# Kernel optimization log

Hardware: AMD Instinct MI355X
Metric: run time of the kernel (lower is better)

## Reference

```python
import jax, jax.numpy as jnp
import numpy as np


def _gelu(x):
    # torch.nn.functional.gelu default: exact erf form
    return jax.nn.gelu(x, approximate=False)


def setup_inputs() -> dict:
    key = jax.random.key(0)
    ks = jax.random.split(key, 6)
    B, L, H, MAXLEN = 8, 2048, 1024, 256
    former_input = jax.random.normal(ks[0], (B, L, H), dtype=jnp.float32)
    hidden_sates = jax.random.normal(ks[1], (B, L, H), dtype=jnp.float32)
    token_type_ids = jax.random.randint(ks[2], (B, L), 0, MAXLEN, dtype=jnp.int32)
    attention_mask = jnp.ones((B, L), dtype=jnp.float32)
    # learned params (init.normal_ std=0.02, biases zero)
    W_down = jax.random.normal(ks[3], (2 * H, H), dtype=jnp.float32) * 0.02
    b_down = jnp.zeros((H,), dtype=jnp.float32)
    W_row = jax.random.normal(ks[4], (H, H), dtype=jnp.float32) * 0.02
    b_row = jnp.zeros((H,), dtype=jnp.float32)
    return {
        "former_input": former_input,
        "hidden_sates": hidden_sates,
        "token_type_ids": token_type_ids,
        "attention_mask": attention_mask,
        "W_down": W_down,
        "b_down": b_down,
        "W_row": W_row,
        "b_row": b_row,
        "max_length": 256,
    }


def reference(former_input, hidden_sates, token_type_ids, attention_mask,
              W_down, b_down, W_row, b_row, max_length):
    # down_proj + gelu: [B, L, 2H] @ [2H, H] -> [B, L, H]
    x = jnp.concatenate([former_input, hidden_sates], axis=-1)
    sequence_output = _gelu(jnp.einsum("blf,fh->blh", x, W_down) + b_down)

    # one_hot_from @ sequence_output == segment-sum of tokens into table cells
    # cell_hidden[b, t] = sum_{l : token_type_ids[b,l]==t} sequence_output[b, l]
    seg = jax.vmap(lambda vals, ids: jax.ops.segment_sum(vals, ids, num_segments=max_length))
    cell_hidden = seg(sequence_output, token_type_ids)  # [B, max_length, H]

    # row_linear + gelu (dropout is identity in eval mode)
    cell_hidden = _gelu(jnp.einsum("bth,hk->btk", cell_hidden, W_row) + b_row)

    # one_hot_to @ cell_hidden == gather cell back to each token position
    seq_hidden = jnp.take_along_axis(
        cell_hidden, token_type_ids[:, :, None].astype(jnp.int32), axis=1
    )  # [B, L, H]
    return seq_hidden
```

## Files before the change

### kernel.cpp

```cpp
#include <hip/hip_runtime.h>

typedef unsigned short ushort_t;
typedef __bf16 bf16x8 __attribute__((ext_vector_type(8)));
typedef float f32x4 __attribute__((ext_vector_type(4)));

__device__ __forceinline__ unsigned short f2bf(float f) {
    unsigned u = __float_as_uint(f);
    u += 0x7fffu + ((u >> 16) & 1u);
    return (unsigned short)(u >> 16);
}
__device__ __forceinline__ float bf2f(unsigned short h) {
    return __uint_as_float(((unsigned)h) << 16);
}
__device__ __forceinline__ float gelu_f(float x) {
    return 0.5f * x * (1.0f + erff(x * 0.70710678118654752440f));
}

__global__ void prep_kernel(const float4* __restrict__ former,
                            const float4* __restrict__ hidden,
                            uint4* __restrict__ Xb4,
                            const float* __restrict__ Wd, ushort_t* __restrict__ WdT,
                            const float* __restrict__ Wr, ushort_t* __restrict__ WrT)
{
    const int blk = blockIdx.x;
    const int tid = threadIdx.x;
    if (blk < 16384) {
        const int row = blk;
        const float4* src = (tid < 128)
            ? (former + (size_t)row * 256 + (tid & 127) * 2)
            : (hidden + (size_t)row * 256 + (tid & 127) * 2);
        float4 a = src[0], b = src[1];
        uint4 o;
        o.x = f2bf(a.x) | ((unsigned)f2bf(a.y) << 16);
        o.y = f2bf(a.z) | ((unsigned)f2bf(a.w) << 16);
        o.z = f2bf(b.x) | ((unsigned)f2bf(b.y) << 16);
        o.w = f2bf(b.z) | ((unsigned)f2bf(b.w) << 16);
        Xb4[(size_t)row * 256 + tid] = o;
    } else {
        __shared__ float tile[32][33];
        const float* W; ushort_t* Wt; int R, C, b;
        if (blk < 16384 + 2048) { b = blk - 16384; W = Wd; Wt = WdT; R = 2048; C = 1024; }
        else                    { b = blk - 18432; W = Wr; Wt = WrT; R = 1024; C = 1024; }
        const int bx = (b & 31) * 32;
        const int by = (b >> 5) * 32;
        const int tx = tid & 31, ty = tid >> 5;
        #pragma unroll
        for (int j = 0; j < 32; j += 8)
            tile[ty + j][tx] = W[(size_t)(by + ty + j) * C + bx + tx];
        __syncthreads();
        #pragma unroll
        for (int j = 0; j < 32; j += 8)
            Wt[(size_t)(bx + ty + j) * R + by + tx] = f2bf(tile[tx][ty + j]);
    }
}

template <bool OUT_BF16>
__global__ void gemm_bias_gelu_kernel(const ushort_t* __restrict__ A,
                                      const ushort_t* __restrict__ Bt,
                                      const float* __restrict__ bias,
                                      void* __restrict__ C,
                                      int M, int N, int K)
{
    __shared__ __align__(16) ushort_t sA[128 * 64];
    __shared__ __align__(16) ushort_t sB[128 * 64];
    const int tid  = threadIdx.x;
    const int lane = tid & 63;
    const int wave = tid >> 6;
    const int wm = (wave & 1) * 64;
    const int wn = (wave >> 1) * 64;
    const long bm = (long)blockIdx.x * 128;
    const long bn = (long)blockIdx.y * 128;

    f32x4 acc[4][4] = {};

    const int srow = wave * 8 + (lane >> 3);
    const int scol = ((lane & 7) ^ (lane >> 3)) * 8;
    const int ldsbase = wave * 512;

    for (int k0 = 0; k0 < K; k0 += 64) {
        __syncthreads();
        #pragma unroll
        for (int it = 0; it < 4; ++it) {
            const ushort_t* gA = A + (size_t)(bm + it * 32 + srow) * K + k0 + scol;
            const ushort_t* gB = Bt + (size_t)(bn + it * 32 + srow) * K + k0 + scol;
            __builtin_amdgcn_global_load_lds(
                (__attribute__((address_space(1))) void*)gA,
                (__attribute__((address_space(3))) void*)&sA[ldsbase + it * 2048], 16, 0, 0);
            __builtin_amdgcn_global_load_lds(
                (__attribute__((address_space(1))) void*)gB,
                (__attribute__((address_space(3))) void*)&sB[ldsbase + it * 2048], 16, 0, 0);
        }
        __syncthreads();

        const int arow = wm + (lane & 15);
        const int brow = wn + (lane & 15);
        const int sw = lane & 7;
        const int cbase = lane >> 4;
        #pragma unroll
        for (int kk = 0; kk < 64; kk += 32) {
            const int koff = (((kk >> 3) + cbase) ^ sw) << 3;
            bf16x8 af[4], bfr[4];
            #pragma unroll
            for (int t = 0; t < 4; ++t) {
                af[t]  = *(const bf16x8*)&sA[(arow + t * 16) * 64 + koff];
                bfr[t] = *(const bf16x8*)&sB[(brow + t * 16) * 64 + koff];
            }
            #pragma unroll
            for (int i = 0; i < 4; ++i)
                #pragma unroll
                for (int j = 0; j < 4; ++j)
                    acc[i][j] = __builtin_amdgcn_mfma_f32_16x16x32_bf16(af[i], bfr[j], acc[i][j], 0, 0, 0);
        }
    }

    #pragma unroll
    for (int i = 0; i < 4; ++i) {
        const long row0 = bm + wm + i * 16 + (lane >> 4) * 4;
        #pragma unroll
        for (int j = 0; j < 4; ++j) {
            const long col = bn + wn + j * 16 + (lane & 15);
            const float bv = bias[col];
            #pragma unroll
            for (int r = 0; r < 4; ++r) {
                float v = gelu_f(acc[i][j][r] + bv);
                if (OUT_BF16)
                    ((ushort_t*)C)[(size_t)(row0 + r) * N + col] = f2bf(v);
                else
                    ((float*)C)[(size_t)(row0 + r) * N + col] = v;
            }
        }
    }
}

__global__ void segsum_kernel(const ushort_t* __restrict__ seq,
                              const int* __restrict__ ids,
                              ushort_t* __restrict__ cell)
{
    const int b = blockIdx.x >> 8;
    const int t = blockIdx.x & 255;
    __shared__ int list[2048];
    __shared__ int count;
    if (threadIdx.x == 0) count = 0;
    __syncthreads();
    const int* idrow = ids + b * 2048;
    for (int l = threadIdx.x; l < 2048; l += 256) {
        if (idrow[l] == t) list[atomicAdd(&count, 1)] = l;
    }
    __syncthreads();
    const int n = count;
    float a0 = 0.f, a1 = 0.f, a2 = 0.f, a3 = 0.f;
    for (int i = 0; i < n; ++i) {
        const int l = list[i];
        const ushort4 v = *(const ushort4*)(seq + (size_t)(b * 2048 + l) * 1024 + threadIdx.x * 4);
        a0 += bf2f(v.x); a1 += bf2f(v.y); a2 += bf2f(v.z); a3 += bf2f(v.w);
    }
    ushort4* out = (ushort4*)(cell + (size_t)(b * 256 + t) * 1024);
    out[threadIdx.x] = make_ushort4(f2bf(a0), f2bf(a1), f2bf(a2), f2bf(a3));
}

__global__ void gather_kernel(const float4* __restrict__ cellout,
                              const int* __restrict__ ids,
                              float4* __restrict__ out)
{
    const int tok = blockIdx.x;
    const int b = tok >> 11;
    const int t = ids[tok];
    out[(size_t)tok * 256 + threadIdx.x] = cellout[(size_t)(b * 256 + t) * 256 + threadIdx.x];
}

extern "C" void kernel_launch(void* const* d_in, const int* in_sizes, int n_in,
                              void* d_out, int out_size, void* d_ws, size_t ws_size,
                              hipStream_t stream) {
    const float* former = (const float*)d_in[0];
    const float* hidden = (const float*)d_in[1];
    const int*   ids    = (const int*)d_in[2];
    const float* W_down = (const float*)d_in[4];
    const float* b_down = (const float*)d_in[5];
    const float* W_row  = (const float*)d_in[6];
    const float* b_row  = (const float*)d_in[7];
    float* out = (float*)d_out;

    char* ws = (char*)d_ws;
    ushort_t* Xb    = (ushort_t*)ws;  ws += (size_t)16384 * 2048 * 2;
    ushort_t* WdT   = (ushort_t*)ws;  ws += (size_t)1024 * 2048 * 2;
    ushort_t* WrT   = (ushort_t*)ws;  ws += (size_t)1024 * 1024 * 2;
    ushort_t* seq   = (ushort_t*)ws;  ws += (size_t)16384 * 1024 * 2;
    ushort_t* cellb = (ushort_t*)ws;  ws += (size_t)2048 * 1024 * 2;
    float*    cello = (float*)ws;

    prep_kernel<<<19456, 256, 0, stream>>>((const float4*)former, (const float4*)hidden,
                                           (uint4*)Xb, W_down, WdT, W_row, WrT);

    gemm_bias_gelu_kernel<true><<<dim3(128, 8), 256, 0, stream>>>(Xb, WdT, b_down, seq,
                                                                  16384, 1024, 2048);
    segsum_kernel<<<2048, 256, 0, stream>>>(seq, ids, cellb);

    gemm_bias_gelu_kernel<false><<<dim3(16, 8), 256, 0, stream>>>(cellb, WrT, b_row, cello,
                                                                  2048, 1024, 1024);
    gather_kernel<<<16384, 256, 0, stream>>>((const float4*)cello, ids, (float4*)out);
}
```

Measured before the change: 320.7 us.

## Replace big down-projection GEMM with 256x256-tile double-buffered pipelined kernel

Adds a new bf16 MFMA GEMM that uses 256x256 output tiles and 8 waves with 128KB of dynamic LDS. The next K tiles are prefetched into a second buffer with global_load_lds, staged in quarters alongside the MFMA work, with explicit vmcnt waits and s_setprio. It replaces the 128x128 single-buffered kernel for the large 16384x1024x2048 down projection, aiming to hide global-load latency and raise data reuse per tile. The costs are much higher register and LDS pressure, which limits occupancy, and only 256 blocks, which may leave some of the CUs underused.

```diff
diff --git a/kernel.cpp b/kernel.cpp
--- a/kernel.cpp
+++ b/kernel.cpp
@@ -132,6 +132,139 @@
     }
 }
 
+template <bool OUT_BF16>
+__global__ __launch_bounds__(512, 2)
+void gemm256_bias_gelu_kernel(const ushort_t* __restrict__ A,
+                              const ushort_t* __restrict__ Bt,
+                              const float* __restrict__ bias,
+                              void* __restrict__ C,
+                              int M, int N, int K)
+{
+    extern __shared__ float4 smem4[];
+    ushort_t* sA = (ushort_t*)smem4;
+    ushort_t* sB = sA + 32768;
+
+    const int tid  = threadIdx.x;
+    const int lane = tid & 63;
+    const int w    = tid >> 6;
+    const int wr   = w >> 2;
+    const int wcq  = w & 3;
+    const long bm = (long)blockIdx.x * 256;
+    const long bn = (long)blockIdx.y * 256;
+    const int NT = K >> 6;
+
+    const int srow = w * 8 + (lane >> 3);
+    const int scol = ((lane & 7) ^ (lane >> 3)) * 8;
+    const int sdst = (lane & 7) * 8;
+
+    const int l15 = lane & 15;
+    const int lg  = lane >> 4;
+    const int sw  = lane & 7;
+    const int ck[2] = { ((0 + lg) ^ sw) * 8, ((4 + lg) ^ sw) * 8 };
+
+    f32x4 acc[8][4] = {};
+
+    auto stageA = [&](int t_, int mh_, int buf_) {
+        #pragma unroll
+        for (int j = 0; j < 2; ++j) {
+            const ushort_t* g = A + (size_t)(bm + j * 128 + mh_ * 64 + srow) * K
+                                  + t_ * 64 + scol;
+            ushort_t* d = sA + buf_ * 16384 + mh_ * 8192 + (j * 64 + srow) * 64 + sdst;
+            __builtin_amdgcn_global_load_lds(
+                (__attribute__((address_space(1))) void*)g,
+                (__attribute__((address_space(3))) void*)d, 16, 0, 0);
+        }
+    };
+    auto stageB = [&](int t_, int nh_, int buf_) {
+        #pragma unroll
+        for (int j = 0; j < 2; ++j) {
+            const ushort_t* g = Bt + (size_t)(bn + (j * 2 + wr) * 64 + nh_ * 32
+                                              + (w & 3) * 8 + (lane >> 3)) * K
+                                   + t_ * 64 + scol;
+            ushort_t* d = sB + buf_ * 16384 + nh_ * 8192 + (j * 64 + srow) * 64 + sdst;
+            __builtin_amdgcn_global_load_lds(
+                (__attribute__((address_space(1))) void*)g,
+                (__attribute__((address_space(3))) void*)d, 16, 0, 0);
+        }
+    };
+
+    stageA(0, 0, 0); stageB(0, 0, 0);
+    stageA(0, 1, 0); stageB(0, 1, 0);
+    stageA(1, 0, 1); stageB(1, 0, 1);
+    asm volatile("s_waitcnt vmcnt(4)" ::: "memory");
+
+    for (int t2 = 0; t2 < NT; t2 += 2) {
+        #pragma unroll
+        for (int hIt = 0; hIt < 2; ++hIt) {
+            const int t = t2 + hIt;
+            const int cur = hIt;
+            const bool lastt = (t == NT - 1);
+            #pragma unroll
+            for (int q = 0; q < 4; ++q) {
+                const int mh = q >> 1, nh = q & 1;
+                if (q == 0) {
+                    if (lastt) asm volatile("s_waitcnt vmcnt(0)" ::: "memory");
+                    else       asm volatile("s_waitcnt vmcnt(8)" ::: "memory");
+                } else if (q == 1 && !lastt) {
+                    asm volatile("s_waitcnt vmcnt(6)" ::: "memory");
+                }
+                __builtin_amdgcn_s_barrier();
+
+                bf16x8 af[4][2], bfr[2][2];
+                #pragma unroll
+                for (int tf = 0; tf < 4; ++tf)
+                    #pragma unroll
+                    for (int kk = 0; kk < 2; ++kk)
+                        af[tf][kk] = *(const bf16x8*)&sA[cur * 16384 + mh * 8192
+                                        + (wr * 64 + tf * 16 + l15) * 64 + ck[kk]];
+                #pragma unroll
+                for (int u = 0; u < 2; ++u)
+                    #pragma unroll
+                    for (int kk = 0; kk < 2; ++kk)
+                        bfr[u][kk] = *(const bf16x8*)&sB[cur * 16384 + nh * 8192
+                                        + (wcq * 32 + u * 16 + l15) * 64 + ck[kk]];
+
+                if      (q == 0) { if (t + 1 < NT) stageA(t + 1, 1, cur ^ 1); }
+                else if (q == 1) { if (t + 1 < NT) stageB(t + 1, 1, cur ^ 1); }
+                else if (q == 2) { if (t + 2 < NT) stageA(t + 2, 0, cur); }
+                else             { if (t + 2 < NT) stageB(t + 2, 0, cur); }
+
+                __builtin_amdgcn_s_setprio(1);
+                #pragma unroll
+                for (int tf = 0; tf < 4; ++tf)
+                    #pragma unroll
+                    for (int u = 0; u < 2; ++u) {
+                        acc[mh * 4 + tf][nh * 2 + u] =
+                            __builtin_amdgcn_mfma_f32_16x16x32_bf16(
+                                af[tf][0], bfr[u][0], acc[mh * 4 + tf][nh * 2 + u], 0, 0, 0);
+                        acc[mh * 4 + tf][nh * 2 + u] =
+                            __builtin_amdgcn_mfma_f32_16x16x32_bf16(
+                                af[tf][1], bfr[u][1], acc[mh * 4 + tf][nh * 2 + u], 0, 0, 0);
+                    }
+                __builtin_amdgcn_s_setprio(0);
+            }
+        }
+    }
+
+    #pragma unroll
+    for (int im = 0; im < 8; ++im) {
+        const long row0 = bm + wr * 128 + (im >> 2) * 64 + (im & 3) * 16 + lg * 4;
+        #pragma unroll
+        for (int jn = 0; jn < 4; ++jn) {
+            const long col = bn + wcq * 64 + jn * 16 + l15;
+            const float bv = bias[col];
+            #pragma unroll
+            for (int r = 0; r < 4; ++r) {
+                float v = gelu_f(acc[im][jn][r] + bv);
+                if (OUT_BF16)
+                    ((ushort_t*)C)[(size_t)(row0 + r) * N + col] = f2bf(v);
+                else
+                    ((float*)C)[(size_t)(row0 + r) * N + col] = v;
+            }
+        }
+    }
+}
+
 __global__ void segsum_kernel(const ushort_t* __restrict__ seq,
                               const int* __restrict__ ids,
                               ushort_t* __restrict__ cell)
@@ -188,11 +321,19 @@
     ushort_t* cellb = (ushort_t*)ws;  ws += (size_t)2048 * 1024 * 2;
     float*    cello = (float*)ws;
 
+    static bool s_attr_set = false;
+    if (!s_attr_set) {
+        hipFuncSetAttribute(reinterpret_cast<const void*>(&gemm256_bias_gelu_kernel<true>),
+                            hipFuncAttributeMaxDynamicSharedMemorySize, 131072);
+        s_attr_set = true;
+    }
+
     prep_kernel<<<19456, 256, 0, stream>>>((const float4*)former, (const float4*)hidden,
                                            (uint4*)Xb, W_down, WdT, W_row, WrT);
 
-    gemm_bias_gelu_kernel<true><<<dim3(128, 8), 256, 0, stream>>>(Xb, WdT, b_down, seq,
-                                                                  16384, 1024, 2048);
+    gemm256_bias_gelu_kernel<true><<<dim3(64, 4), 512, 131072, stream>>>(
+        Xb, WdT, b_down, seq, 16384, 1024, 2048);
+
     segsum_kernel<<<2048, 256, 0, stream>>>(seq, ids, cellb);
 
     gemm_bias_gelu_kernel<false><<<dim3(16, 8), 256, 0, stream>>>(cellb, WrT, b_row, cello,
```

Result: no change. 325.6 us (+1.5%).

## Fuse fp32-to-bf16 conversion of activations into the first GEMM's A-tile load

Applied to the files above, without the earlier changes.

The separate pass that converted and concatenated former/hidden inputs into a bf16 buffer is removed. The first GEMM now reads fp32 activations straight from the two inputs, picking the source by K offset, converts them in registers, and writes them into the swizzled LDS tile. The next A tile is prefetched into registers while the MFMAs run. This drops a 64MB write and re-read of the bf16 buffer. In exchange, each GEMM block re-reads fp32 A once per N tile, which is 8x redundant and twice the bytes, and register pressure goes up.

```diff
diff --git a/kernel.cpp b/kernel.cpp
--- a/kernel.cpp
+++ b/kernel.cpp
@@ -16,41 +16,117 @@
     return 0.5f * x * (1.0f + erff(x * 0.70710678118654752440f));
 }
 
-__global__ void prep_kernel(const float4* __restrict__ former,
-                            const float4* __restrict__ hidden,
-                            uint4* __restrict__ Xb4,
-                            const float* __restrict__ Wd, ushort_t* __restrict__ WdT,
-                            const float* __restrict__ Wr, ushort_t* __restrict__ WrT)
-{
+__global__ void prep_transpose_kernel(const float* __restrict__ Wd, ushort_t* __restrict__ WdT,
+                                      const float* __restrict__ Wr, ushort_t* __restrict__ WrT)
+{
+    __shared__ float tile[32][33];
     const int blk = blockIdx.x;
     const int tid = threadIdx.x;
-    if (blk < 16384) {
-        const int row = blk;
-        const float4* src = (tid < 128)
-            ? (former + (size_t)row * 256 + (tid & 127) * 2)
-            : (hidden + (size_t)row * 256 + (tid & 127) * 2);
-        float4 a = src[0], b = src[1];
-        uint4 o;
-        o.x = f2bf(a.x) | ((unsigned)f2bf(a.y) << 16);
-        o.y = f2bf(a.z) | ((unsigned)f2bf(a.w) << 16);
-        o.z = f2bf(b.x) | ((unsigned)f2bf(b.y) << 16);
-        o.w = f2bf(b.z) | ((unsigned)f2bf(b.w) << 16);
-        Xb4[(size_t)row * 256 + tid] = o;
-    } else {
-        __shared__ float tile[32][33];
-        const float* W; ushort_t* Wt; int R, C, b;
-        if (blk < 16384 + 2048) { b = blk - 16384; W = Wd; Wt = WdT; R = 2048; C = 1024; }
-        else                    { b = blk - 18432; W = Wr; Wt = WrT; R = 1024; C = 1024; }
-        const int bx = (b & 31) * 32;
-        const int by = (b >> 5) * 32;
-        const int tx = tid & 31, ty = tid >> 5;
-        #pragma unroll
-        for (int j = 0; j < 32; j += 8)
-            tile[ty + j][tx] = W[(size_t)(by + ty + j) * C + bx + tx];
-        __syncthreads();
-        #pragma unroll
-        for (int j = 0; j < 32; j += 8)
-            Wt[(size_t)(bx + ty + j) * R + by + tx] = f2bf(tile[tx][ty + j]);
+    const float* W; ushort_t* Wt; int R, C, b;
+    if (blk < 2048) { b = blk;        W = Wd; Wt = WdT; R = 2048; C = 1024; }
+    else            { b = blk - 2048; W = Wr; Wt = WrT; R = 1024; C = 1024; }
+    const int bx = (b & 31) * 32;
+    const int by = (b >> 5) * 32;
+    const int tx = tid & 31, ty = tid >> 5;
+    #pragma unroll
+    for (int j = 0; j < 32; j += 8)
+        tile[ty + j][tx] = W[(size_t)(by + ty + j) * C + bx + tx];
+    __syncthreads();
+    #pragma unroll
+    for (int j = 0; j < 32; j += 8)
+        Wt[(size_t)(bx + ty + j) * R + by + tx] = f2bf(tile[tx][ty + j]);
+}
+
+__global__ __launch_bounds__(256)
+void gemm1_fused_kernel(const float* __restrict__ Af,
+                        const float* __restrict__ Ah,
+                        const ushort_t* __restrict__ Bt,
+                        const float* __restrict__ bias,
+                        ushort_t* __restrict__ C)
+{
+    const int N = 1024, K = 2048;
+    __shared__ __align__(16) ushort_t sA[128 * 64];
+    __shared__ __align__(16) ushort_t sB[128 * 64];
+    const int tid  = threadIdx.x;
+    const int lane = tid & 63;
+    const int wave = tid >> 6;
+    const int wm = (wave & 1) * 64;
+    const int wn = (wave >> 1) * 64;
+    const long bm = (long)blockIdx.x * 128;
+    const long bn = (long)blockIdx.y * 128;
+
+    f32x4 acc[4][4] = {};
+
+    const int srow = wave * 8 + (lane >> 3);
+    const int scol = ((lane & 7) ^ (lane >> 3)) * 8;
+    const int ldsbase = wave * 512;
+
+    float4 fa[4][2];
+    auto loadA = [&](int k0) {
+        const float* Abase = (k0 < 1024) ? Af : Ah;
+        const int koff = (k0 & 1023) + scol;
+        #pragma unroll
+        for (int it = 0; it < 4; ++it) {
+            const float* g = Abase + (size_t)(bm + it * 32 + srow) * 1024 + koff;
+            fa[it][0] = *(const float4*)g;
+            fa[it][1] = *(const float4*)(g + 4);
+        }
+    };
+
+    loadA(0);
+    for (int k0 = 0; k0 < K; k0 += 64) {
+        __syncthreads();
+        #pragma unroll
+        for (int it = 0; it < 4; ++it) {
+            bf16x8 v;
+            #pragma unroll
+            for (int e = 0; e < 4; ++e) {
+                v[e]     = (__bf16)((&fa[it][0].x)[e]);
+                v[e + 4] = (__bf16)((&fa[it][1].x)[e]);
+            }
+            *(bf16x8*)&sA[ldsbase + it * 2048 + lane * 8] = v;
+            const ushort_t* gB = Bt + (size_t)(bn + it * 32 + srow) * K + k0 + scol;
+            __builtin_amdgcn_global_load_lds(
+                (__attribute__((address_space(1))) void*)gB,
+                (__attribute__((address_space(3))) void*)&sB[ldsbase + it * 2048], 16, 0, 0);
+        }
+        __syncthreads();
+        if (k0 + 64 < K) loadA(k0 + 64);
+
+        const int arow = wm + (lane & 15);
+        const int brow = wn + (lane & 15);
+        const int sw = lane & 7;
+        const int cbase = lane >> 4;
+        #pragma unroll
+        for (int kk = 0; kk < 64; kk += 32) {
+            const int koff2 = (((kk >> 3) + cbase) ^ sw) << 3;
+            bf16x8 af[4], bfr[4];
+            #pragma unroll
+            for (int t = 0; t < 4; ++t) {
+                af[t]  = *(const bf16x8*)&sA[(arow + t * 16) * 64 + koff2];
+                bfr[t] = *(const bf16x8*)&sB[(brow + t * 16) * 64 + koff2];
+            }
+            #pragma unroll
+            for (int i = 0; i < 4; ++i)
+                #pragma unroll
+                for (int j = 0; j < 4; ++j)
+                    acc[i][j] = __builtin_amdgcn_mfma_f32_16x16x32_bf16(af[i], bfr[j], acc[i][j], 0, 0, 0);
+        }
+    }
+
+    #pragma unroll
+    for (int i = 0; i < 4; ++i) {
+        const long row0 = bm + wm + i * 16 + (lane >> 4) * 4;
+        #pragma unroll
+        for (int j = 0; j < 4; ++j) {
+            const long col = bn + wn + j * 16 + (lane & 15);
+            const float bv = bias[col];
+            #pragma unroll
+            for (int r = 0; r < 4; ++r) {
+                float v = gelu_f(acc[i][j][r] + bv);
+                C[(size_t)(row0 + r) * N + col] = f2bf(v);
+            }
+        }
     }
 }
 
@@ -181,18 +257,16 @@
     float* out = (float*)d_out;
 
     char* ws = (char*)d_ws;
-    ushort_t* Xb    = (ushort_t*)ws;  ws += (size_t)16384 * 2048 * 2;
     ushort_t* WdT   = (ushort_t*)ws;  ws += (size_t)1024 * 2048 * 2;
     ushort_t* WrT   = (ushort_t*)ws;  ws += (size_t)1024 * 1024 * 2;
     ushort_t* seq   = (ushort_t*)ws;  ws += (size_t)16384 * 1024 * 2;
     ushort_t* cellb = (ushort_t*)ws;  ws += (size_t)2048 * 1024 * 2;
     float*    cello = (float*)ws;
 
-    prep_kernel<<<19456, 256, 0, stream>>>((const float4*)former, (const float4*)hidden,
-                                           (uint4*)Xb, W_down, WdT, W_row, WrT);
-
-    gemm_bias_gelu_kernel<true><<<dim3(128, 8), 256, 0, stream>>>(Xb, WdT, b_down, seq,
-                                                                  16384, 1024, 2048);
+    prep_transpose_kernel<<<3072, 256, 0, stream>>>(W_down, WdT, W_row, WrT);
+
+    gemm1_fused_kernel<<<dim3(128, 8), 256, 0, stream>>>(former, hidden, WdT, b_down, seq);
+
     segsum_kernel<<<2048, 256, 0, stream>>>(seq, ids, cellb);
 
     gemm_bias_gelu_kernel<false><<<dim3(16, 8), 256, 0, stream>>>(cellb, WrT, b_row, cello,
```

New measurement: 334.6 us. +4.3%, slower.
